# Performance work log

Hardware: AMD Instinct MI355X
Metric: run time of the kernel (lower is better)

Reference implementation:

```python
import jax, jax.numpy as jnp
import numpy as np

R, C = 30, 56
N = R * C  # 1680
K = 0.005
PRCN = 15
ALPHA = 1.0
BETA = 1.0


def setup_inputs() -> dict:
    key = jax.random.key(0)
    k1, k2 = jax.random.split(key)
    net_in = jax.random.normal(k1, (2 * N,), dtype=jnp.float32)
    # Recurrent connectivity matrix (learned weight in the original, loaded from .mat)
    J = jax.random.normal(k2, (N, N), dtype=jnp.float32) / np.float32(np.sqrt(N))
    return {"net_in": net_in, "J": J}


def reference(net_in, J):
    Iext = net_in[:N].reshape(R, C)
    r0 = net_in[N:2 * N].reshape(R, C)

    def step(r, _):
        # 4-way chunked mm + cat in the original == single matvec J @ r_flat
        temp = (J @ r.reshape(N)).reshape(R, C)
        U = ALPHA * (BETA * temp) + ALPHA * Iext
        sq = jnp.square(0.2 * U)
        recSum = jnp.sum(K * sq)
        # (0.2*U)^2 * (0.04 / recSum) / 0.04  ==  sq / recSum, kept explicit for fidelity
        r_new = sq * (0.04 / recSum) / 0.04
        return r_new, (U, recSum)

    r_last, (Us, sums) = jax.lax.scan(step, r0, None, length=PRCN - 1)
    return Us[-1], sums[-1], r_last
```

## Files before the change

kernel.cpp:

```cpp
#include <hip/hip_runtime.h>


#define N 1680
#define NV4 420
#define NBLK 420
#define NSTEP 14

__global__ __launch_bounds__(256) void step_kernel(
    const float* __restrict__ J,
    const float* __restrict__ net_in,
    const float* __restrict__ r_prev,
    float* __restrict__ r_new,
    const float* __restrict__ partials_prev,
    float* __restrict__ partials_cur,
    float* __restrict__ d_out,
    int first, int last)
{
    __shared__ float r_lds[N];
    __shared__ float sred[4];
    __shared__ float wsq[4];

    const int tid  = threadIdx.x;
    const int lane = tid & 63;
    const int wave = tid >> 6;

    const float4* rp4 = (const float4*)r_prev;
    float4* rl4 = (float4*)r_lds;
    for (int i = tid; i < NV4; i += 256) rl4[i] = rp4[i];

    float p = 0.0f;
    if (!first) {
        for (int i = tid; i < NBLK; i += 256) p += partials_prev[i];
    }
    #pragma unroll
    for (int off = 32; off; off >>= 1) p += __shfl_xor(p, off, 64);
    if (lane == 0) sred[wave] = p;
    __syncthreads();
    const float s_prev = first ? 1.0f : (sred[0] + sred[1] + sred[2] + sred[3]);

    const int row = blockIdx.x * 4 + wave;
    const float4* Jrow = (const float4*)(J + (size_t)row * N);
    float acc = 0.0f;
    #pragma unroll
    for (int k = 0; k < 7; ++k) {
        const int idx = lane + 64 * k;
        if (idx < NV4) {
            const float4 a = Jrow[idx];
            const float4 b = rl4[idx];
            acc += a.x * b.x + a.y * b.y + a.z * b.z + a.w * b.w;
        }
    }
    #pragma unroll
    for (int off = 32; off; off >>= 1) acc += __shfl_xor(acc, off, 64);

    if (lane == 0) {
        const float U  = acc / s_prev + net_in[row];
        const float u2 = 0.2f * U;
        const float sq = u2 * u2;
        r_new[row] = sq;
        if (last) d_out[row] = U;
        wsq[wave] = 0.005f * sq;
    }
    __syncthreads();
    if (tid == 0) partials_cur[blockIdx.x] = wsq[0] + wsq[1] + wsq[2] + wsq[3];
}

__global__ __launch_bounds__(256) void finish_kernel(
    const float* __restrict__ r_last_un,
    const float* __restrict__ partials_last,
    float* __restrict__ d_out)
{
    __shared__ float sred[4];
    const int tid  = threadIdx.x;
    const int lane = tid & 63;
    const int wave = tid >> 6;

    float p = 0.0f;
    for (int i = tid; i < NBLK; i += 256) p += partials_last[i];
    #pragma unroll
    for (int off = 32; off; off >>= 1) p += __shfl_xor(p, off, 64);
    if (lane == 0) sred[wave] = p;
    __syncthreads();
    const float s = sred[0] + sred[1] + sred[2] + sred[3];

    const int gid = blockIdx.x * 256 + tid;
    if (gid == 0) d_out[N] = s;
    if (gid < N) d_out[N + 1 + gid] = r_last_un[gid] / s;
}

extern "C" void kernel_launch(void* const* d_in, const int* in_sizes, int n_in,
                              void* d_out, int out_size, void* d_ws, size_t ws_size,
                              hipStream_t stream) {
    const float* net_in = (const float*)d_in[0];
    const float* J      = (const float*)d_in[1];
    float* out = (float*)d_out;
    float* ws  = (float*)d_ws;

    float* rbuf[2] = { ws, ws + 1792 };
    float* partials = ws + 3584;

    const float* r_prev = net_in + N;
    for (int t = 0; t < NSTEP; ++t) {
        float* r_new = rbuf[t & 1];
        const float* pp = (t == 0) ? nullptr : partials + (size_t)(t - 1) * NBLK;
        float* pc = partials + (size_t)t * NBLK;
        step_kernel<<<NBLK, 256, 0, stream>>>(J, net_in, r_prev, r_new, pp, pc,
                                              out, t == 0 ? 1 : 0, t == NSTEP - 1 ? 1 : 0);
        r_prev = r_new;
    }
    finish_kernel<<<7, 256, 0, stream>>>(r_prev, partials + (size_t)(NSTEP - 1) * NBLK, out);
}
```

Baseline: 120.5 us.

## Fuse all recurrence steps into one persistent cooperative kernel with register-resident J

Replaces 15 kernel launches (14 step kernels plus a finish kernel) with a single cooperative persistent kernel of 70 blocks × 512 threads. Each wave keeps three rows of J in registers across all steps, and steps are separated by an atomic grid barrier. Partial sums are double-buffered. The aim is to remove per-launch overhead and the repeated reads of J from global memory. In exchange it adds grid-barrier spin latency, uses many registers per thread, and relies on all 70 blocks being co-resident.

```diff
diff --git a/kernel.cpp b/kernel.cpp
--- a/kernel.cpp
+++ b/kernel.cpp
@@ -3,89 +3,137 @@
 
 #define N 1680
 #define NV4 420
-#define NBLK 420
+#define NV4_PAD 448
+#define NBLK 70
+#define BLOCK 512
+#define WAVES 8
+#define RPW 3
 #define NSTEP 14
 
-__global__ __launch_bounds__(256) void step_kernel(
+__device__ __forceinline__ float wave_reduce(float v) {
+    #pragma unroll
+    for (int off = 32; off; off >>= 1) v += __shfl_xor(v, off, 64);
+    return v;
+}
+
+__device__ __forceinline__ void grid_barrier(unsigned* cnt, unsigned target) {
+    __syncthreads();
+    if (threadIdx.x == 0) {
+        __threadfence();
+        __hip_atomic_fetch_add(cnt, 1u, __ATOMIC_RELEASE, __HIP_MEMORY_SCOPE_AGENT);
+        while (__hip_atomic_load(cnt, __ATOMIC_ACQUIRE, __HIP_MEMORY_SCOPE_AGENT) < target) {
+            __builtin_amdgcn_s_sleep(1);
+        }
+        __threadfence();
+    }
+    __syncthreads();
+}
+
+__global__ __launch_bounds__(BLOCK) void cann_persistent(
     const float* __restrict__ J,
     const float* __restrict__ net_in,
-    const float* __restrict__ r_prev,
-    float* __restrict__ r_new,
-    const float* __restrict__ partials_prev,
-    float* __restrict__ partials_cur,
     float* __restrict__ d_out,
-    int first, int last)
+    unsigned* __restrict__ cnt,
+    float* __restrict__ rbuf0, float* __restrict__ rbuf1,
+    float* __restrict__ part0, float* __restrict__ part1)
 {
-    __shared__ float r_lds[N];
-    __shared__ float sred[4];
-    __shared__ float wsq[4];
+    __shared__ float r_lds[NV4_PAD * 4];
+    __shared__ float wsum[WAVES];
 
     const int tid  = threadIdx.x;
     const int lane = tid & 63;
     const int wave = tid >> 6;
+    const int gw   = blockIdx.x * WAVES + wave;
+    const int row0 = gw * RPW;
 
-    const float4* rp4 = (const float4*)r_prev;
-    float4* rl4 = (float4*)r_lds;
-    for (int i = tid; i < NV4; i += 256) rl4[i] = rp4[i];
-
-    float p = 0.0f;
-    if (!first) {
-        for (int i = tid; i < NBLK; i += 256) p += partials_prev[i];
-    }
+    float4 Jreg[RPW][7];
     #pragma unroll
-    for (int off = 32; off; off >>= 1) p += __shfl_xor(p, off, 64);
-    if (lane == 0) sred[wave] = p;
-    __syncthreads();
-    const float s_prev = first ? 1.0f : (sred[0] + sred[1] + sred[2] + sred[3]);
-
-    const int row = blockIdx.x * 4 + wave;
-    const float4* Jrow = (const float4*)(J + (size_t)row * N);
-    float acc = 0.0f;
-    #pragma unroll
-    for (int k = 0; k < 7; ++k) {
-        const int idx = lane + 64 * k;
-        if (idx < NV4) {
-            const float4 a = Jrow[idx];
-            const float4 b = rl4[idx];
-            acc += a.x * b.x + a.y * b.y + a.z * b.z + a.w * b.w;
+    for (int r = 0; r < RPW; ++r) {
+        const float4* Jrow = (const float4*)(J + (size_t)(row0 + r) * N);
+        #pragma unroll
+        for (int k = 0; k < 7; ++k) {
+            const int idx = lane + 64 * k;
+            Jreg[r][k] = (idx < NV4) ? Jrow[idx] : make_float4(0.f, 0.f, 0.f, 0.f);
         }
     }
-    #pragma unroll
-    for (int off = 32; off; off >>= 1) acc += __shfl_xor(acc, off, 64);
+    float iext[RPW];
+    if (lane == 0) {
+        #pragma unroll
+        for (int r = 0; r < RPW; ++r) iext[r] = net_in[row0 + r];
+    }
 
-    if (lane == 0) {
-        const float U  = acc / s_prev + net_in[row];
-        const float u2 = 0.2f * U;
-        const float sq = u2 * u2;
-        r_new[row] = sq;
-        if (last) d_out[row] = U;
-        wsq[wave] = 0.005f * sq;
+    float sqv[RPW];
+
+    for (int t = 0; t < NSTEP; ++t) {
+        float s_prev = 1.0f;
+        if (t > 0) {
+            const float* pp = ((t - 1) & 1) ? part1 : part0;
+            float p = pp[lane];
+            if (lane < NBLK - 64) p += pp[64 + lane];
+            s_prev = wave_reduce(p);
+        }
+
+        const float* rsrc = (t == 0) ? (net_in + N) : (((t - 1) & 1) ? rbuf1 : rbuf0);
+        {
+            float4* rl4 = (float4*)r_lds;
+            const float4* rp4 = (const float4*)rsrc;
+            for (int i = tid; i < NV4_PAD; i += BLOCK)
+                rl4[i] = (i < NV4) ? rp4[i] : make_float4(0.f, 0.f, 0.f, 0.f);
+        }
+        __syncthreads();
+
+        const float4* rl4 = (const float4*)r_lds;
+        float acc[RPW];
+        #pragma unroll
+        for (int r = 0; r < RPW; ++r) {
+            float a = 0.f;
+            #pragma unroll
+            for (int k = 0; k < 7; ++k) {
+                const float4 jv = Jreg[r][k];
+                const float4 rv = rl4[lane + 64 * k];
+                a += jv.x * rv.x + jv.y * rv.y + jv.z * rv.z + jv.w * rv.w;
+            }
+            acc[r] = wave_reduce(a);
+        }
+
+        float psum = 0.f;
+        if (lane == 0) {
+            float* rdst = (t & 1) ? rbuf1 : rbuf0;
+            #pragma unroll
+            for (int r = 0; r < RPW; ++r) {
+                const float U  = acc[r] / s_prev + iext[r];
+                const float u2 = 0.2f * U;
+                const float sq = u2 * u2;
+                sqv[r] = sq;
+                rdst[row0 + r] = sq;
+                psum += sq;
+                if (t == NSTEP - 1) d_out[row0 + r] = U;
+            }
+            wsum[wave] = 0.005f * psum;
+        }
+        __syncthreads();
+        if (tid == 0) {
+            float bp = 0.f;
+            #pragma unroll
+            for (int w = 0; w < WAVES; ++w) bp += wsum[w];
+            float* pc = (t & 1) ? part1 : part0;
+            pc[blockIdx.x] = bp;
+        }
+
+        grid_barrier(cnt, (unsigned)((t + 1) * NBLK));
     }
-    __syncthreads();
-    if (tid == 0) partials_cur[blockIdx.x] = wsq[0] + wsq[1] + wsq[2] + wsq[3];
-}
 
-__global__ __launch_bounds__(256) void finish_kernel(
-    const float* __restrict__ r_last_un,
-    const float* __restrict__ partials_last,
-    float* __restrict__ d_out)
-{
-    __shared__ float sred[4];
-    const int tid  = threadIdx.x;
-    const int lane = tid & 63;
-    const int wave = tid >> 6;
-
-    float p = 0.0f;
-    for (int i = tid; i < NBLK; i += 256) p += partials_last[i];
-    #pragma unroll
-    for (int off = 32; off; off >>= 1) p += __shfl_xor(p, off, 64);
-    if (lane == 0) sred[wave] = p;
-    __syncthreads();
-    const float s = sred[0] + sred[1] + sred[2] + sred[3];
-
-    const int gid = blockIdx.x * 256 + tid;
-    if (gid == 0) d_out[N] = s;
-    if (gid < N) d_out[N + 1 + gid] = r_last_un[gid] / s;
+    {
+        float p = part1[lane];
+        if (lane < NBLK - 64) p += part1[64 + lane];
+        const float s = wave_reduce(p);
+        if (lane == 0) {
+            if (blockIdx.x == 0 && wave == 0) d_out[N] = s;
+            #pragma unroll
+            for (int r = 0; r < RPW; ++r)
+                d_out[N + 1 + row0 + r] = sqv[r] / s;
+        }
+    }
 }
 
 extern "C" void kernel_launch(void* const* d_in, const int* in_sizes, int n_in,
@@ -96,17 +144,16 @@
     float* out = (float*)d_out;
     float* ws  = (float*)d_ws;
 
-    float* rbuf[2] = { ws, ws + 1792 };
-    float* partials = ws + 3584;
+    unsigned* cnt = (unsigned*)ws;
+    float* rbuf0 = ws + 64;
+    float* rbuf1 = ws + 64 + 1728;
+    float* part0 = ws + 64 + 3456;
+    float* part1 = part0 + 70;
 
-    const float* r_prev = net_in + N;
-    for (int t = 0; t < NSTEP; ++t) {
-        float* r_new = rbuf[t & 1];
-        const float* pp = (t == 0) ? nullptr : partials + (size_t)(t - 1) * NBLK;
-        float* pc = partials + (size_t)t * NBLK;
-        step_kernel<<<NBLK, 256, 0, stream>>>(J, net_in, r_prev, r_new, pp, pc,
-                                              out, t == 0 ? 1 : 0, t == NSTEP - 1 ? 1 : 0);
-        r_prev = r_new;
-    }
-    finish_kernel<<<7, 256, 0, stream>>>(r_prev, partials + (size_t)(NSTEP - 1) * NBLK, out);
+    hipMemsetAsync(cnt, 0, sizeof(unsigned), stream);
+
+    void* args[] = { (void*)&J, (void*)&net_in, (void*)&out, (void*)&cnt,
+                     (void*)&rbuf0, (void*)&rbuf1, (void*)&part0, (void*)&part1 };
+    hipLaunchCooperativeKernel((void*)cann_persistent, dim3(NBLK), dim3(BLOCK),
+                               args, 0, stream);
 }
```

After: 195.1 us. 1.62x slower.
